# Performance work log

Measured on AMD Instinct MI355X. Metric: run time of the kernel, lower is better.

The kernel has to match this reference:

```python
import jax, jax.numpy as jnp
import numpy as np

N_OUT = 8      # outer experts
INNER = 2      # inner experts per outer expert
E = N_OUT * INNER  # 16 total experts
ACTI = 2       # outer top-k (acti_num)
PATTERN = (2, 1)   # inner top-k per outer slot (acti_pattern)
D = 1024       # hidden_dim
F = 512        # expert ffn dim
B, S = 1, 1024


def setup_inputs() -> dict:
    key = jax.random.key(0)
    ks = jax.random.split(key, 6)
    w = lambda k, shape: jax.random.normal(k, shape, jnp.float32) * 0.02
    return {
        "hidden_states": jax.random.normal(ks[0], (B, S, D), jnp.float32),
        "w_out_gate": w(ks[1], (N_OUT, D)),
        "w_in_gates": w(ks[2], (N_OUT, INNER, D)),
        "w_gate_proj": w(ks[3], (E, F, D)),
        "w_up_proj": w(ks[4], (E, F, D)),
        "w_down_proj": w(ks[5], (E, D, F)),
    }


def reference(hidden_states, w_out_gate, w_in_gates, w_gate_proj, w_up_proj, w_down_proj):
    Bb, Ss, Dd = hidden_states.shape
    x = hidden_states.reshape(-1, Dd)          # [T, D]
    T = x.shape[0]

    # --- RouterCompound: outer gate ---
    logits = x @ w_out_gate.T                  # [T, n_out]
    probs = jax.nn.softmax(logits.astype(jnp.float32), axis=-1)
    rw, sel = jax.lax.top_k(probs, ACTI)       # [T, A] weights, outer expert ids
    rw = rw / rw.sum(axis=-1, keepdims=True)   # norm_topk_prob=True

    # --- inner gates: score all (outer, inner) pairs, gather selected outer ---
    inner_all = jnp.einsum('td,oid->toi', x, w_in_gates)           # [T, n_out, inner]
    inner_sel = jnp.take_along_axis(inner_all, sel[:, :, None], axis=1)  # [T, A, inner]
    max_k = max(PATTERN)
    _, top_idx = jax.lax.top_k(inner_sel, max_k)                   # [T, A, max_k]
    flat_ids = sel[:, :, None] * INNER + top_idx                   # global expert ids
    # per outer slot j keep first PATTERN[j] inner experts (static pattern)
    sel_ids = jnp.concatenate([flat_ids[:, j, :p] for j, p in enumerate(PATTERN)], axis=1)  # [T, K]
    sel_w = jnp.concatenate([jnp.repeat(rw[:, j:j + 1], p, axis=1) for j, p in enumerate(PATTERN)], axis=1)  # [T, K]
    sel_w = sel_w.astype(x.dtype)

    # --- dispatch/combine: dense masked combine (math-identical to index_add loop) ---
    combine = jnp.zeros((T, E), x.dtype).at[jnp.arange(T)[:, None], sel_ids].add(sel_w)  # [T, E]
    g = jnp.einsum('td,efd->tef', x, w_gate_proj)   # [T, E, F]
    u = jnp.einsum('td,efd->tef', x, w_up_proj)
    h = jax.nn.silu(g) * u                          # SwiGLU activation
    y = jnp.einsum('tef,edf->ted', h, w_down_proj)  # [T, E, D]
    out = jnp.einsum('ted,te->td', y, combine)      # weighted combine
    return out.reshape(Bb, Ss, Dd), sel_w
```

## Files before the change

kernel.cpp:

```cpp
#include <hip/hip_runtime.h>
#include <hip/hip_bf16.h>

typedef __bf16 bf16_t;
typedef __bf16 bf16x8 __attribute__((ext_vector_type(8)));
typedef float floatx4 __attribute__((ext_vector_type(4)));
typedef unsigned int u32;

#define T_TOK 1024
#define DIM   1024
#define FF    512
#define NEXP  16

#define FLAG_OFF 0
#define CNT_OFF  64
#define TOK_OFF  256
#define SEL_OFF  65792
#define H_OFF    78080
#define XBF_OFF  (H_OFF + (size_t)3072*512*2)
#define WGB_OFF  (XBF_OFF + (size_t)T_TOK*DIM*2)
#define WUB_OFF  (WGB_OFF + (size_t)NEXP*FF*DIM*2)
#define WDB_OFF  (WUB_OFF + (size_t)NEXP*FF*DIM*2)
#define Y_OFF    (WDB_OFF + (size_t)NEXP*DIM*FF*2)
#define WS_FULL  (Y_OFF + (size_t)3072*DIM*4)

__device__ inline float swiglu(float g, float u) {
    float a = fminf(fmaxf(-g, -60.f), 60.f);
    return g * u / (1.0f + __expf(a));
}

__device__ __forceinline__ void gload_lds16(const void* g, void* l) {
    __builtin_amdgcn_global_load_lds((const __attribute__((address_space(1))) u32*)g,
                                     (__attribute__((address_space(3))) u32*)l, 16, 0, 0);
}

template<int N> __device__ __forceinline__ void waitv() {
    asm volatile("s_waitcnt vmcnt(%0)" :: "n"(N) : "memory");
}
__device__ __forceinline__ void barrier_raw() { __builtin_amdgcn_s_barrier(); }

__device__ __forceinline__ bf16x8 cvt8(float4 a, float4 b) {
    bf16x8 r;
    r[0]=(bf16_t)a.x; r[1]=(bf16_t)a.y; r[2]=(bf16_t)a.z; r[3]=(bf16_t)a.w;
    r[4]=(bf16_t)b.x; r[5]=(bf16_t)b.y; r[6]=(bf16_t)b.z; r[7]=(bf16_t)b.w;
    return r;
}

__device__ __forceinline__ bf16x8 rdT(const char* L, int r, int q) {
    return *(const bf16x8*)(L + r * 128 + ((q ^ (r & 7)) << 4));
}

__device__ inline bf16x8 loadB8r(const void* base, size_t off, bool f32) {
    if (f32) {
        const float4* p = (const float4*)((const float*)base + off);
        return cvt8(p[0], p[1]);
    } else {
        return *(const bf16x8*)((const bf16_t*)base + off);
    }
}

__device__ int blk_f32(const void* p, int tid, int* tmp) {
    const unsigned short* h = (const unsigned short*)p;
    unsigned bad = 0;
    for (int i = tid; i < 4096; i += 256) {
        unsigned e = ((unsigned)h[i] >> 7) & 0xFFu;
        if (e >= 0x90u) bad = 1;
    }
    unsigned long long bl = __ballot(bad != 0);
    __syncthreads();
    if ((tid & 63) == 0) tmp[tid >> 6] = (bl != 0ull) ? 1 : 0;
    __syncthreads();
    return tmp[0] | tmp[1] | tmp[2] | tmp[3];
}

__global__ __launch_bounds__(256) void prep2_kernel(
    const void* __restrict__ x, const void* __restrict__ w_out, const void* __restrict__ w_in,
    const void* __restrict__ wg, const void* __restrict__ wu, const void* __restrict__ wd,
    float* __restrict__ selw_out, int* __restrict__ sel_ids,
    bf16_t* __restrict__ xb, int* __restrict__ flags,
    bf16_t* __restrict__ wgb, bf16_t* __restrict__ wub, bf16_t* __restrict__ wdb)
{
    const int b = blockIdx.x;
    const int tid = threadIdx.x;
    __shared__ int tmp[4];
    __shared__ float Ls[24];

    if (b >= T_TOK + 6) {
        const int c = b - (T_TOK + 6);
        const int z = c >> 12, i = c & 4095;
        const void* src; bf16_t* dst;
        if (z == 0)      { src = wg; dst = wgb; }
        else if (z == 1) { src = wu; dst = wub; }
        else             { src = wd; dst = wdb; }
        const unsigned short* h = (const unsigned short*)src;
        unsigned bad = 0;
        for (int k = tid; k < 4096; k += 256) {
            unsigned ex = ((unsigned)h[k] >> 7) & 0xFFu;
            if (ex >= 0x90u) bad = 1;
        }
        unsigned long long bl = __ballot(bad != 0);
        if ((tid & 63) == 0) tmp[tid >> 6] = (bl != 0ull) ? 1 : 0;
        __syncthreads();
        if (!(tmp[0] | tmp[1] | tmp[2] | tmp[3])) return;
        size_t off = ((size_t)i * 256 + tid) * 8;
        const float4* p = (const float4*)((const float*)src + off);
        float4 a = p[0], bb = p[1];
        *(bf16x8*)(dst + off) = cvt8(a, bb);
        return;
    }

    if (b >= T_TOK) {
        const int j = b - T_TOK;
        const void* ps[6] = {x, w_out, w_in, wg, wu, wd};
        const unsigned short* h = (const unsigned short*)ps[j];
        unsigned bad = 0;
        for (int i = tid; i < 4096; i += 256) {
            unsigned e = ((unsigned)h[i] >> 7) & 0xFFu;
            if (e >= 0x90u) bad = 1;
        }
        unsigned long long bl = __ballot(bad != 0);
        if ((tid & 63) == 0) tmp[tid >> 6] = (bl != 0ull) ? 1 : 0;
        __syncthreads();
        if (tid == 0) flags[j] = tmp[0] | tmp[1] | tmp[2] | tmp[3];
        return;
    }

    const bool xf  = blk_f32(x, tid, tmp) != 0;
    const bool gof = blk_f32(w_out, tid, tmp) != 0;
    const bool gif = blk_f32(w_in, tid, tmp) != 0;

    const int wave = tid >> 6, lane = tid & 63;
    const int t = b;

    float xv[16];
    if (xf) {
        const float* xp = (const float*)x + (size_t)t * DIM;
        #pragma unroll
        for (int i = 0; i < 16; i++) xv[i] = xp[lane + 64 * i];
    } else {
        const bf16_t* xp = (const bf16_t*)x + (size_t)t * DIM;
        #pragma unroll
        for (int i = 0; i < 16; i++) xv[i] = (float)xp[lane + 64 * i];
    }

    if (wave == 0 && xb) {
        #pragma unroll
        for (int i = 0; i < 16; i++)
            xb[(size_t)t * DIM + lane + 64 * i] = (bf16_t)xv[i];
    }

    #pragma unroll
    for (int jj = 0; jj < 6; jj++) {
        const int j = wave * 6 + jj;
        const void* gb; int row; bool gf;
        if (j < 8) { gb = w_out; row = j;     gf = gof; }
        else       { gb = w_in;  row = j - 8; gf = gif; }
        float s = 0.f;
        if (gf) {
            const float* gp = (const float*)gb + (size_t)row * DIM;
            #pragma unroll
            for (int i = 0; i < 16; i++) s += xv[i] * gp[lane + 64 * i];
        } else {
            const bf16_t* gp = (const bf16_t*)gb + (size_t)row * DIM;
            #pragma unroll
            for (int i = 0; i < 16; i++) s += xv[i] * (float)gp[lane + 64 * i];
        }
        #pragma unroll
        for (int m = 32; m >= 1; m >>= 1) s += __shfl_xor(s, m, 64);
        if (lane == 0) Ls[j] = s;
    }
    __syncthreads();

    if (tid == 0) {
        const float* logits = Ls;
        float mx = logits[0];
        for (int o = 1; o < 8; o++) mx = fmaxf(mx, logits[o]);
        float p[8];
        for (int o = 0; o < 8; o++) p[o] = __expf(logits[o] - mx);
        int i0 = 0;
        for (int o = 1; o < 8; o++) if (logits[o] > logits[i0]) i0 = o;
        int i1 = (i0 == 0) ? 1 : 0;
        for (int o = 0; o < 8; o++) if (o != i0 && logits[o] > logits[i1]) i1 = o;
        float rsum = p[i0] + p[i1];
        float rw0 = p[i0] / rsum, rw1 = p[i1] / rsum;

        float a0 = logits[8 + i0 * 2], a1 = logits[8 + i0 * 2 + 1];
        int j00 = (a1 > a0) ? 1 : 0;
        float b0 = logits[8 + i1 * 2], b1 = logits[8 + i1 * 2 + 1];
        int j10 = (b1 > b0) ? 1 : 0;

        int   ids[3] = { i0 * 2 + j00, i0 * 2 + (1 - j00), i1 * 2 + j10 };
        float w[3]   = { rw0, rw0, rw1 };

        #pragma unroll
        for (int k = 0; k < 3; k++) {
            selw_out[t * 3 + k] = w[k];
            sel_ids[t * 3 + k]  = ids[k];
        }
    }
}

__global__ __launch_bounds__(1024) void bin2_kernel(
    const int* __restrict__ sel_ids,
    int* __restrict__ cnt, int* __restrict__ tok_enc)
{
    const int e = blockIdx.x, tid = threadIdx.x;
    const int wave = tid >> 6, lane = tid & 63;
    __shared__ int wbase[16];

    int my = -1;
    #pragma unroll
    for (int k = 0; k < 3; k++) {
        int id = sel_ids[tid * 3 + k];
        if (id == e) my = tid | (k << 16);
    }
    unsigned long long b = __ballot(my >= 0);
    if (lane == 0) wbase[wave] = __popcll(b);
    __syncthreads();
    if (tid == 0) {
        int s = 0;
        for (int w = 0; w < 16; w++) { int c = wbase[w]; wbase[w] = s; s += c; }
        cnt[e] = s;
    }
    __syncthreads();
    if (my >= 0) {
        int pos = wbase[wave] + __popcll(b & ((1ull << lane) - 1ull));
        if (pos < T_TOK) tok_enc[e * T_TOK + pos] = my;
    }
}


__global__ __launch_bounds__(512, 4) void gateup5_kernel(
    const bf16_t* __restrict__ xb,
    const void* __restrict__ wg, const void* __restrict__ wu,
    const bf16_t* __restrict__ wgb, const bf16_t* __restrict__ wub,
    const int* __restrict__ flags, const int* __restrict__ cnt,
    const int* __restrict__ tok_enc, bf16_t* __restrict__ H)
{
    __shared__ __align__(16) char Xs[3 * 16384];
    __shared__ __align__(16) char Gs[3 * 4096];
    __shared__ __align__(16) char Us[3 * 4096];
    __shared__ int toks[128];
    __shared__ int hrow[128];

    const int ft = blockIdx.x, mt = blockIdx.y, e = blockIdx.z;
    int C = cnt[e]; if (C > T_TOK) C = T_TOK; if (C < 0) C = 0;
    if (mt * 128 >= C) return;

    const bf16_t* wgp = (flags[3] != 0) ? wgb : (const bf16_t*)wg;
    const bf16_t* wup = (flags[4] != 0) ? wub : (const bf16_t*)wu;

    const int tid = threadIdx.x;
    if (tid < 128) {
        int idx = mt * 128 + tid, t = 0, hr = -1;
        if (idx < C) {
            int enc = tok_enc[e * T_TOK + idx];
            int tt = enc & 0xFFFF, kk = (enc >> 16) & 0xFFFF;
            if (tt < T_TOK && kk < 3) { t = tt; hr = tt * 3 + kk; }
        }
        toks[tid] = t; hrow[tid] = hr;
    }
    __syncthreads();

    const int wave = tid >> 6, lane = tid & 63;
    const int mh = wave >> 1, fq = wave & 1;
    const int rsel = lane & 15, kq = lane >> 4;

    constexpr int NC  = 16;
    constexpr int PER = 3;

    const bf16_t* px[2];
    #pragma unroll
    for (int j = 0; j < 2; j++) {
        int n = (2 * wave + j) * 64 + lane, r = n >> 3, s = n & 7;
        px[j] = xb + (size_t)toks[r] * DIM + ((s ^ (r & 7)) << 3);
    }
    const bf16_t* pw;
    {
        int wv = wave & 3;
        int n = wv * 64 + lane, r = n >> 3, s = n & 7;
        int row = e * FF + ft * 32 + r;
        pw = (wave < 4 ? wgp : wup) + (size_t)row * DIM + ((s ^ (r & 7)) << 3);
    }
    char* wdst = (wave < 4 ? Gs : Us);
    const int wslot = (wave & 3) * 1024;

    auto issue = [&](int kc) {
        const int buf = kc % 3;
        gload_lds16(px[0] + kc * 64, Xs + buf * 16384 + (2 * wave) * 1024);
        gload_lds16(px[1] + kc * 64, Xs + buf * 16384 + (2 * wave + 1) * 1024);
        gload_lds16(pw + kc * 64, wdst + buf * 4096 + wslot);
    };

    floatx4 ag[2], au[2];
    #pragma unroll
    for (int ms = 0; ms < 2; ms++) { ag[ms] = (floatx4){0,0,0,0}; au[ms] = (floatx4){0,0,0,0}; }

    issue(0);
    issue(1);

    #pragma unroll
    for (int kc = 0; kc < NC; kc++) {
        if (kc + 2 < NC) issue(kc + 2);
        if (kc + 2 < NC)      waitv<2 * PER>();
        else if (kc + 1 < NC) waitv<PER>();
        else                  waitv<0>();
        barrier_raw();
        __builtin_amdgcn_sched_barrier(0);

        const char* X = Xs + (kc % 3) * 16384;
        const char* G = Gs + (kc % 3) * 4096;
        const char* U = Us + (kc % 3) * 4096;
        #pragma unroll
        for (int i = 0; i < 2; i++) {
            const int q = i * 4 + kq;
            bf16x8 a0 = rdT(X, mh * 32 + rsel, q);
            bf16x8 a1 = rdT(X, mh * 32 + 16 + rsel, q);
            bf16x8 bg = rdT(G, fq * 16 + rsel, q);
            bf16x8 bu = rdT(U, fq * 16 + rsel, q);
            ag[0] = __builtin_amdgcn_mfma_f32_16x16x32_bf16(a0, bg, ag[0], 0, 0, 0);
            au[0] = __builtin_amdgcn_mfma_f32_16x16x32_bf16(a0, bu, au[0], 0, 0, 0);
            ag[1] = __builtin_amdgcn_mfma_f32_16x16x32_bf16(a1, bg, ag[1], 0, 0, 0);
            au[1] = __builtin_amdgcn_mfma_f32_16x16x32_bf16(a1, bu, au[1], 0, 0, 0);
        }
        barrier_raw();
    }

    const int f = ft * 32 + fq * 16 + rsel;
    #pragma unroll
    for (int ms = 0; ms < 2; ms++)
        #pragma unroll
        for (int r = 0; r < 4; r++) {
            int m = mh * 32 + ms * 16 + kq * 4 + r;
            int hr = hrow[m];
            if (hr >= 0)
                H[(size_t)hr * FF + f] = (bf16_t)swiglu(ag[ms][r], au[ms][r]);
        }
}

__global__ __launch_bounds__(512, 4) void down5_kernel(
    const void* __restrict__ wd, const bf16_t* __restrict__ wdb,
    const int* __restrict__ flags, const int* __restrict__ cnt,
    const int* __restrict__ tok_enc,
    const bf16_t* __restrict__ H, float* __restrict__ Y)
{
    __shared__ __align__(16) char Hs[3 * 16384];
    __shared__ __align__(16) char Ds[3 * 8192];
    __shared__ int hsrc[128];
    __shared__ int hdst[128];

    const int dt = blockIdx.x, mt = blockIdx.y, e = blockIdx.z;
    int C = cnt[e]; if (C > T_TOK) C = T_TOK; if (C < 0) C = 0;
    if (mt * 128 >= C) return;

    const bf16_t* wdp = (flags[5] != 0) ? wdb : (const bf16_t*)wd;

    const int tid = threadIdx.x;
    if (tid < 128) {
        int idx = mt * 128 + tid, hr = -1;
        if (idx < C) {
            int enc = tok_enc[e * T_TOK + idx];
            int tt = enc & 0xFFFF, kk = (enc >> 16) & 0xFFFF;
            if (tt < T_TOK && kk < 3) hr = tt * 3 + kk;
        }
        hsrc[tid] = (hr >= 0) ? hr : 0;
        hdst[tid] = hr;
    }
    __syncthreads();

    const int wave = tid >> 6, lane = tid & 63;
    const int mh = wave >> 1, dq = wave & 1;
    const int rsel = lane & 15, kq = lane >> 4;

    constexpr int NC  = 8;
    constexpr int PER = 3;

    const bf16_t* ph[2];
    #pragma unroll
    for (int j = 0; j < 2; j++) {
        int n = (2 * wave + j) * 64 + lane, r = n >> 3, s = n & 7;
        ph[j] = H + (size_t)hsrc[r] * FF + ((s ^ (r & 7)) << 3);
    }
    const bf16_t* pd;
    {
        int n = wave * 64 + lane, r = n >> 3, s = n & 7;
        int row = e * DIM + dt * 64 + r;
        pd = wdp + (size_t)row * FF + ((s ^ (r & 7)) << 3);
    }

    auto issue = [&](int kc) {
        const int buf = kc % 3;
        gload_lds16(ph[0] + kc * 64, Hs + buf * 16384 + (2 * wave) * 1024);
        gload_lds16(ph[1] + kc * 64, Hs + buf * 16384 + (2 * wave + 1) * 1024);
        gload_lds16(pd + kc * 64, Ds + buf * 8192 + wave * 1024);
    };

    floatx4 acc[2][2];
    #pragma unroll
    for (int ms = 0; ms < 2; ms++)
        #pragma unroll
        for (int nt = 0; nt < 2; nt++) acc[ms][nt] = (floatx4){0,0,0,0};

    issue(0);
    issue(1);

    #pragma unroll
    for (int kc = 0; kc < NC; kc++) {
        if (kc + 2 < NC) issue(kc + 2);
        if (kc + 2 < NC)      waitv<2 * PER>();
        else if (kc + 1 < NC) waitv<PER>();
        else                  waitv<0>();
        barrier_raw();
        __builtin_amdgcn_sched_barrier(0);

        const char* Hb = Hs + (kc % 3) * 16384;
        const char* Db = Ds + (kc % 3) * 8192;
        #pragma unroll
        for (int i = 0; i < 2; i++) {
            const int q = i * 4 + kq;
            bf16x8 a0 = rdT(Hb, mh * 32 + rsel, q);
            bf16x8 a1 = rdT(Hb, mh * 32 + 16 + rsel, q);
            bf16x8 b0 = rdT(Db, dq * 32 + rsel, q);
            bf16x8 b1 = rdT(Db, dq * 32 + 16 + rsel, q);
            acc[0][0] = __builtin_amdgcn_mfma_f32_16x16x32_bf16(a0, b0, acc[0][0], 0, 0, 0);
            acc[0][1] = __builtin_amdgcn_mfma_f32_16x16x32_bf16(a0, b1, acc[0][1], 0, 0, 0);
            acc[1][0] = __builtin_amdgcn_mfma_f32_16x16x32_bf16(a1, b0, acc[1][0], 0, 0, 0);
            acc[1][1] = __builtin_amdgcn_mfma_f32_16x16x32_bf16(a1, b1, acc[1][1], 0, 0, 0);
        }
        barrier_raw();
    }

    #pragma unroll
    for (int ms = 0; ms < 2; ms++)
        #pragma unroll
        for (int nt = 0; nt < 2; nt++)
            #pragma unroll
            for (int r = 0; r < 4; r++) {
                int m = mh * 32 + ms * 16 + kq * 4 + r;
                int hr = hdst[m];
                if (hr >= 0)
                    Y[(size_t)hr * DIM + dt * 64 + dq * 32 + nt * 16 + rsel] = acc[ms][nt][r];
            }
}

__global__ __launch_bounds__(256) void combine_kernel(
    const float* __restrict__ Y, const float* __restrict__ selw,
    float* __restrict__ outp)
{
    int idx = blockIdx.x * 256 + threadIdx.x;
    int t = idx >> 8;
    int d = (idx & 255) * 4;
    float w0 = selw[t * 3 + 0], w1 = selw[t * 3 + 1], w2 = selw[t * 3 + 2];
    float4 y0 = *(const float4*)(Y + (size_t)(t * 3 + 0) * DIM + d);
    float4 y1 = *(const float4*)(Y + (size_t)(t * 3 + 1) * DIM + d);
    float4 y2 = *(const float4*)(Y + (size_t)(t * 3 + 2) * DIM + d);
    float4 o;
    o.x = w0 * y0.x + w1 * y1.x + w2 * y2.x;
    o.y = w0 * y0.y + w1 * y1.y + w2 * y2.y;
    o.z = w0 * y0.z + w1 * y1.z + w2 * y2.z;
    o.w = w0 * y0.w + w1 * y1.w + w2 * y2.w;
    *(float4*)(outp + (size_t)t * DIM + d) = o;
}

__global__ __launch_bounds__(256) void ffn_kernel(
    const void* __restrict__ x,
    const void* __restrict__ wg, const void* __restrict__ wu, const void* __restrict__ wd,
    const int* __restrict__ flags, const int* __restrict__ cnt, const int* __restrict__ tok_enc,
    const float* __restrict__ selw, float* __restrict__ outp)
{
    const int e = blockIdx.x, tile = blockIdx.y;
    int C = cnt[e]; if (C > T_TOK) C = T_TOK; if (C < 0) C = 0;
    if (tile * 16 >= C) return;
    const bool xf = flags[0] != 0, gf = flags[3] != 0, uf = flags[4] != 0, df = flags[5] != 0;

    __shared__ __align__(16) bf16_t Xs[16][1032];
    __shared__ __align__(16) bf16_t Hs[16][520];
    __shared__ int toks[16];
    __shared__ float wts[16];
    const int tid = threadIdx.x;
    if (tid < 16) {
        int idx = tile * 16 + tid, t = -1; float w = 0.f;
        if (idx < C) {
            int enc = tok_enc[e * T_TOK + idx];
            int tt = enc & 0xFFFF, kk = (enc >> 16) & 0xFFFF;
            if (tt < T_TOK && kk < 3) { t = tt; w = selw[tt * 3 + kk]; }
        }
        toks[tid] = t; wts[tid] = w;
    }
    __syncthreads();
    {
        int row = tid >> 4, chunk = tid & 15;
        int t = toks[row];
        bf16x8* dst = (bf16x8*)&Xs[row][chunk * 64];
        if (t >= 0) {
            #pragma unroll
            for (int i = 0; i < 8; i++)
                dst[i] = loadB8r(x, (size_t)t * DIM + chunk * 64 + i * 8, xf);
        } else {
            bf16x8 z;
            #pragma unroll
            for (int kz = 0; kz < 8; kz++) z[kz] = (bf16_t)0.0f;
            #pragma unroll
            for (int i = 0; i < 8; i++) dst[i] = z;
        }
    }
    __syncthreads();

    const int wave = tid >> 6, lane = tid & 63;
    const int rsel = lane & 15, kq = lane >> 4;
    const size_t eoffF = (size_t)e * FF * DIM;
    for (int nt = 0; nt < 8; nt++) {
        const int f0 = wave * 128 + nt * 16;
        const size_t boff = eoffF + (size_t)(f0 + rsel) * DIM + kq * 8;
        const bf16_t* ap = &Xs[rsel][kq * 8];
        floatx4 accg = {0.f,0.f,0.f,0.f};
        floatx4 accu = {0.f,0.f,0.f,0.f};
        for (int k0 = 0; k0 < DIM; k0 += 32) {
            bf16x8 a  = *(const bf16x8*)(ap + k0);
            bf16x8 bg = loadB8r(wg, boff + k0, gf);
            bf16x8 bu = loadB8r(wu, boff + k0, uf);
            accg = __builtin_amdgcn_mfma_f32_16x16x32_bf16(a, bg, accg, 0, 0, 0);
            accu = __builtin_amdgcn_mfma_f32_16x16x32_bf16(a, bu, accu, 0, 0, 0);
        }
        #pragma unroll
        for (int r = 0; r < 4; r++)
            Hs[kq * 4 + r][f0 + rsel] = (bf16_t)swiglu(accg[r], accu[r]);
    }
    __syncthreads();
    const size_t eoffD = (size_t)e * DIM * FF;
    for (int nt = 0; nt < 16; nt++) {
        const int d0 = wave * 256 + nt * 16;
        const size_t boff = eoffD + (size_t)(d0 + rsel) * FF + kq * 8;
        const bf16_t* ap = &Hs[rsel][kq * 8];
        floatx4 acc = {0.f,0.f,0.f,0.f};
        for (int k0 = 0; k0 < FF; k0 += 32) {
            bf16x8 a = *(const bf16x8*)(ap + k0);
            bf16x8 b = loadB8r(wd, boff + k0, df);
            acc = __builtin_amdgcn_mfma_f32_16x16x32_bf16(a, b, acc, 0, 0, 0);
        }
        #pragma unroll
        for (int r = 0; r < 4; r++) {
            int m = kq * 4 + r, t = toks[m];
            if (t >= 0) atomicAdd(outp + (size_t)t * DIM + d0 + rsel, acc[r] * wts[m]);
        }
    }
}

extern "C" void kernel_launch(void* const* d_in, const int* in_sizes, int n_in,
                              void* d_out, int out_size, void* d_ws, size_t ws_size,
                              hipStream_t stream)
{
    const void* x     = d_in[0];
    const void* w_out = d_in[1];
    const void* w_in  = d_in[2];
    const void* wg    = d_in[3];
    const void* wu    = d_in[4];
    const void* wd    = d_in[5];
    float* out  = (float*)d_out;
    float* selw = out + (size_t)T_TOK * DIM;

    char* ws = (char*)d_ws;
    int*    flags = (int*)(ws + FLAG_OFF);
    int*    cnt   = (int*)(ws + CNT_OFF);
    int*    tok   = (int*)(ws + TOK_OFF);
    int*    sel   = (int*)(ws + SEL_OFF);
    bf16_t* H     = (bf16_t*)(ws + H_OFF);
    bf16_t* xbf   = (bf16_t*)(ws + XBF_OFF);
    bf16_t* wgb   = (bf16_t*)(ws + WGB_OFF);
    bf16_t* wub   = (bf16_t*)(ws + WUB_OFF);
    bf16_t* wdb   = (bf16_t*)(ws + WDB_OFF);
    float*  Y     = (float*)(ws + Y_OFF);

    const bool full = ws_size >= (size_t)WS_FULL;

    if (!full)
        hipMemsetAsync(out, 0, (size_t)T_TOK * DIM * sizeof(float), stream);

    const int nblk = (T_TOK + 6) + (full ? 3 * 4096 : 0);
    prep2_kernel<<<dim3(nblk), dim3(256), 0, stream>>>(
        x, w_out, w_in, wg, wu, wd, selw, sel,
        full ? xbf : (bf16_t*)nullptr, flags, wgb, wub, wdb);

    bin2_kernel<<<dim3(NEXP), dim3(1024), 0, stream>>>(sel, cnt, tok);

    if (full) {
        gateup5_kernel<<<dim3(16, 8, 16), dim3(512), 0, stream>>>(
            xbf, wg, wu, wgb, wub, flags, cnt, tok, H);
        down5_kernel<<<dim3(16, 8, 16), dim3(512), 0, stream>>>(
            wd, wdb, flags, cnt, tok, H, Y);
        combine_kernel<<<dim3(T_TOK * DIM / 1024), dim3(256), 0, stream>>>(Y, selw, out);
    } else {
        ffn_kernel<<<dim3(NEXP, 64), dim3(256), 0, stream>>>(
            x, wg, wu, wd, flags, cnt, tok, selw, out);
    }
}
```

Before: 191.8 us.

## Load fp32 expert weights directly into LDS and convert at fragment read time

Drops the separate pass that converted fp32 gate/up/down weights to bf16 copies in the workspace. The GEMM kernels now stream fp32 weights straight into LDS with a 16-way XOR swizzle and convert to bf16 while reading MFMA fragments, with the path picked per dtype through template specialisation. Pipelining goes from triple to double buffering to fit the larger fp32 tiles in LDS. Format detection moves into a small kernel of its own ahead of the router. This removes a full read and write of all weights each call, but gives up one stage of prefetch depth and adds conversion work inside the inner loop.

```diff
diff --git a/kernel.cpp b/kernel.cpp
--- a/kernel.cpp
+++ b/kernel.cpp
@@ -17,10 +17,7 @@
 #define SEL_OFF  65792
 #define H_OFF    78080
 #define XBF_OFF  (H_OFF + (size_t)3072*512*2)
-#define WGB_OFF  (XBF_OFF + (size_t)T_TOK*DIM*2)
-#define WUB_OFF  (WGB_OFF + (size_t)NEXP*FF*DIM*2)
-#define WDB_OFF  (WUB_OFF + (size_t)NEXP*FF*DIM*2)
-#define Y_OFF    (WDB_OFF + (size_t)NEXP*DIM*FF*2)
+#define Y_OFF    (XBF_OFF + (size_t)T_TOK*DIM*2)
 #define WS_FULL  (Y_OFF + (size_t)3072*DIM*4)
 
 __device__ inline float swiglu(float g, float u) {
@@ -47,6 +44,17 @@
 
 __device__ __forceinline__ bf16x8 rdT(const char* L, int r, int q) {
     return *(const bf16x8*)(L + r * 128 + ((q ^ (r & 7)) << 4));
+}
+template<bool F32>
+__device__ __forceinline__ bf16x8 rdW(const char* L, int r, int q) {
+    if constexpr (F32) {
+        const float* p = (const float*)(L + r * 256);
+        float4 a = *(const float4*)(p + ((((2 * q)    ) ^ (r & 15)) << 2));
+        float4 b = *(const float4*)(p + ((((2 * q) + 1) ^ (r & 15)) << 2));
+        return cvt8(a, b);
+    } else {
+        return *(const bf16x8*)(L + r * 128 + ((q ^ (r & 7)) << 4));
+    }
 }
 
 __device__ inline bf16x8 loadB8r(const void* base, size_t off, bool f32) {
@@ -58,78 +66,41 @@
     }
 }
 
-__device__ int blk_f32(const void* p, int tid, int* tmp) {
-    const unsigned short* h = (const unsigned short*)p;
-    unsigned bad = 0;
-    for (int i = tid; i < 4096; i += 256) {
-        unsigned e = ((unsigned)h[i] >> 7) & 0xFFu;
+__global__ __launch_bounds__(64) void detect_kernel(
+    const void* p0, const void* p1, const void* p2,
+    const void* p3, const void* p4, const void* p5,
+    int* __restrict__ flags)
+{
+    const void* ps[6] = {p0, p1, p2, p3, p4, p5};
+    int j = blockIdx.x;
+    int lane = threadIdx.x;
+    const unsigned short* h = (const unsigned short*)ps[j];
+    unsigned int bad = 0;
+    for (int i = lane; i < 4096; i += 64) {
+        unsigned int e = ((unsigned int)h[i] >> 7) & 0xFFu;
         if (e >= 0x90u) bad = 1;
     }
-    unsigned long long bl = __ballot(bad != 0);
-    __syncthreads();
-    if ((tid & 63) == 0) tmp[tid >> 6] = (bl != 0ull) ? 1 : 0;
-    __syncthreads();
-    return tmp[0] | tmp[1] | tmp[2] | tmp[3];
-}
-
-__global__ __launch_bounds__(256) void prep2_kernel(
-    const void* __restrict__ x, const void* __restrict__ w_out, const void* __restrict__ w_in,
-    const void* __restrict__ wg, const void* __restrict__ wu, const void* __restrict__ wd,
-    float* __restrict__ selw_out, int* __restrict__ sel_ids,
-    bf16_t* __restrict__ xb, int* __restrict__ flags,
-    bf16_t* __restrict__ wgb, bf16_t* __restrict__ wub, bf16_t* __restrict__ wdb)
-{
-    const int b = blockIdx.x;
+    unsigned long long b = __ballot(bad);
+    if (lane == 0) flags[j] = (b != 0ull) ? 1 : 0;
+}
+
+__global__ __launch_bounds__(256) void router4_kernel(
+    const void* __restrict__ x,
+    const void* __restrict__ w_out,
+    const void* __restrict__ w_in,
+    float* __restrict__ selw_out,
+    const int* __restrict__ flags,
+    int* __restrict__ sel_ids,
+    bf16_t* __restrict__ xb)
+{
+    const bool xf  = flags[0] != 0;
+    const bool gof = flags[1] != 0;
+    const bool gif = flags[2] != 0;
     const int tid = threadIdx.x;
-    __shared__ int tmp[4];
+    const int wave = tid >> 6, lane = tid & 63;
+    const int t = blockIdx.x;
+
     __shared__ float Ls[24];
-
-    if (b >= T_TOK + 6) {
-        const int c = b - (T_TOK + 6);
-        const int z = c >> 12, i = c & 4095;
-        const void* src; bf16_t* dst;
-        if (z == 0)      { src = wg; dst = wgb; }
-        else if (z == 1) { src = wu; dst = wub; }
-        else             { src = wd; dst = wdb; }
-        const unsigned short* h = (const unsigned short*)src;
-        unsigned bad = 0;
-        for (int k = tid; k < 4096; k += 256) {
-            unsigned ex = ((unsigned)h[k] >> 7) & 0xFFu;
-            if (ex >= 0x90u) bad = 1;
-        }
-        unsigned long long bl = __ballot(bad != 0);
-        if ((tid & 63) == 0) tmp[tid >> 6] = (bl != 0ull) ? 1 : 0;
-        __syncthreads();
-        if (!(tmp[0] | tmp[1] | tmp[2] | tmp[3])) return;
-        size_t off = ((size_t)i * 256 + tid) * 8;
-        const float4* p = (const float4*)((const float*)src + off);
-        float4 a = p[0], bb = p[1];
-        *(bf16x8*)(dst + off) = cvt8(a, bb);
-        return;
-    }
-
-    if (b >= T_TOK) {
-        const int j = b - T_TOK;
-        const void* ps[6] = {x, w_out, w_in, wg, wu, wd};
-        const unsigned short* h = (const unsigned short*)ps[j];
-        unsigned bad = 0;
-        for (int i = tid; i < 4096; i += 256) {
-            unsigned e = ((unsigned)h[i] >> 7) & 0xFFu;
-            if (e >= 0x90u) bad = 1;
-        }
-        unsigned long long bl = __ballot(bad != 0);
-        if ((tid & 63) == 0) tmp[tid >> 6] = (bl != 0ull) ? 1 : 0;
-        __syncthreads();
-        if (tid == 0) flags[j] = tmp[0] | tmp[1] | tmp[2] | tmp[3];
-        return;
-    }
-
-    const bool xf  = blk_f32(x, tid, tmp) != 0;
-    const bool gof = blk_f32(w_out, tid, tmp) != 0;
-    const bool gif = blk_f32(w_in, tid, tmp) != 0;
-
-    const int wave = tid >> 6, lane = tid & 63;
-    const int t = b;
 
     float xv[16];
     if (xf) {
@@ -229,25 +200,17 @@
 }
 
 
-__global__ __launch_bounds__(512, 4) void gateup5_kernel(
+template<bool GF, bool UF>
+__device__ __forceinline__ void gateup6_body(
     const bf16_t* __restrict__ xb,
     const void* __restrict__ wg, const void* __restrict__ wu,
-    const bf16_t* __restrict__ wgb, const bf16_t* __restrict__ wub,
-    const int* __restrict__ flags, const int* __restrict__ cnt,
-    const int* __restrict__ tok_enc, bf16_t* __restrict__ H)
-{
-    __shared__ __align__(16) char Xs[3 * 16384];
-    __shared__ __align__(16) char Gs[3 * 4096];
-    __shared__ __align__(16) char Us[3 * 4096];
-    __shared__ int toks[128];
-    __shared__ int hrow[128];
-
+    const int* __restrict__ cnt, const int* __restrict__ tok_enc,
+    bf16_t* __restrict__ H,
+    char* Xs, char* Gs, char* Us, int* toks, int* hrow)
+{
     const int ft = blockIdx.x, mt = blockIdx.y, e = blockIdx.z;
     int C = cnt[e]; if (C > T_TOK) C = T_TOK; if (C < 0) C = 0;
     if (mt * 128 >= C) return;
-
-    const bf16_t* wgp = (flags[3] != 0) ? wgb : (const bf16_t*)wg;
-    const bf16_t* wup = (flags[4] != 0) ? wub : (const bf16_t*)wu;
 
     const int tid = threadIdx.x;
     if (tid < 128) {
@@ -265,8 +228,12 @@
     const int mh = wave >> 1, fq = wave & 1;
     const int rsel = lane & 15, kq = lane >> 4;
 
-    constexpr int NC  = 16;
-    constexpr int PER = 3;
+    constexpr int NC = 16;
+    constexpr int GSTR = GF ? 8192 : 4096;
+    constexpr int USTR = UF ? 8192 : 4096;
+    constexpr int PG = 2 + (GF ? 2 : 1);
+    constexpr int PU = 2 + (UF ? 2 : 1);
+    const int wrow0 = e * FF + ft * 32;
 
     const bf16_t* px[2];
     #pragma unroll
@@ -274,21 +241,50 @@
         int n = (2 * wave + j) * 64 + lane, r = n >> 3, s = n & 7;
         px[j] = xb + (size_t)toks[r] * DIM + ((s ^ (r & 7)) << 3);
     }
-    const bf16_t* pw;
-    {
-        int wv = wave & 3;
-        int n = wv * 64 + lane, r = n >> 3, s = n & 7;
-        int row = e * FF + ft * 32 + r;
-        pw = (wave < 4 ? wgp : wup) + (size_t)row * DIM + ((s ^ (r & 7)) << 3);
-    }
-    char* wdst = (wave < 4 ? Gs : Us);
-    const int wslot = (wave & 3) * 1024;
+    const int wv = wave & 3;
+    const void* pw0; const void* pw1 = nullptr;
+    char* wdst;
+    int woff0, woff1 = 0;
+    if (wave < 4) {
+        wdst = Gs;
+        if constexpr (GF) {
+            int n0 = (2 * wv) * 64 + lane, r0 = n0 >> 4, s0 = n0 & 15;
+            int n1 = (2 * wv + 1) * 64 + lane, r1 = n1 >> 4, s1 = n1 & 15;
+            pw0 = (const float*)wg + (size_t)(wrow0 + r0) * DIM + ((s0 ^ (r0 & 15)) << 2);
+            pw1 = (const float*)wg + (size_t)(wrow0 + r1) * DIM + ((s1 ^ (r1 & 15)) << 2);
+            woff0 = (2 * wv) * 1024; woff1 = (2 * wv + 1) * 1024;
+        } else {
+            int n = wv * 64 + lane, r = n >> 3, s = n & 7;
+            pw0 = (const bf16_t*)wg + (size_t)(wrow0 + r) * DIM + ((s ^ (r & 7)) << 3);
+            woff0 = wv * 1024;
+        }
+    } else {
+        wdst = Us;
+        if constexpr (UF) {
+            int n0 = (2 * wv) * 64 + lane, r0 = n0 >> 4, s0 = n0 & 15;
+            int n1 = (2 * wv + 1) * 64 + lane, r1 = n1 >> 4, s1 = n1 & 15;
+            pw0 = (const float*)wu + (size_t)(wrow0 + r0) * DIM + ((s0 ^ (r0 & 15)) << 2);
+            pw1 = (const float*)wu + (size_t)(wrow0 + r1) * DIM + ((s1 ^ (r1 & 15)) << 2);
+            woff0 = (2 * wv) * 1024; woff1 = (2 * wv + 1) * 1024;
+        } else {
+            int n = wv * 64 + lane, r = n >> 3, s = n & 7;
+            pw0 = (const bf16_t*)wu + (size_t)(wrow0 + r) * DIM + ((s ^ (r & 7)) << 3);
+            woff0 = wv * 1024;
+        }
+    }
+    const bool wf = (wave < 4) ? GF : UF;
+    const int wstr = (wave < 4) ? GSTR : USTR;
 
     auto issue = [&](int kc) {
-        const int buf = kc % 3;
+        const int buf = kc & 1;
         gload_lds16(px[0] + kc * 64, Xs + buf * 16384 + (2 * wave) * 1024);
         gload_lds16(px[1] + kc * 64, Xs + buf * 16384 + (2 * wave + 1) * 1024);
-        gload_lds16(pw + kc * 64, wdst + buf * 4096 + wslot);
+        if (wf) {
+            gload_lds16((const float*)pw0 + kc * 64, wdst + buf * wstr + woff0);
+            gload_lds16((const float*)pw1 + kc * 64, wdst + buf * wstr + woff1);
+        } else {
+            gload_lds16((const bf16_t*)pw0 + kc * 64, wdst + buf * wstr + woff0);
+        }
     };
 
     floatx4 ag[2], au[2];
@@ -296,27 +292,28 @@
     for (int ms = 0; ms < 2; ms++) { ag[ms] = (floatx4){0,0,0,0}; au[ms] = (floatx4){0,0,0,0}; }
 
     issue(0);
-    issue(1);
 
     #pragma unroll
     for (int kc = 0; kc < NC; kc++) {
-        if (kc + 2 < NC) issue(kc + 2);
-        if (kc + 2 < NC)      waitv<2 * PER>();
-        else if (kc + 1 < NC) waitv<PER>();
-        else                  waitv<0>();
+        if (kc + 1 < NC) {
+            issue(kc + 1);
+            if (wave < 4) waitv<PG>(); else waitv<PU>();
+        } else {
+            waitv<0>();
+        }
         barrier_raw();
         __builtin_amdgcn_sched_barrier(0);
 
-        const char* X = Xs + (kc % 3) * 16384;
-        const char* G = Gs + (kc % 3) * 4096;
-        const char* U = Us + (kc % 3) * 4096;
+        const char* X = Xs + (kc & 1) * 16384;
+        const char* G = Gs + (kc & 1) * GSTR;
+        const char* U = Us + (kc & 1) * USTR;
         #pragma unroll
         for (int i = 0; i < 2; i++) {
             const int q = i * 4 + kq;
             bf16x8 a0 = rdT(X, mh * 32 + rsel, q);
             bf16x8 a1 = rdT(X, mh * 32 + 16 + rsel, q);
-            bf16x8 bg = rdT(G, fq * 16 + rsel, q);
-            bf16x8 bu = rdT(U, fq * 16 + rsel, q);
+            bf16x8 bg = rdW<GF>(G, fq * 16 + rsel, q);
+            bf16x8 bu = rdW<UF>(U, fq * 16 + rsel, q);
             ag[0] = __builtin_amdgcn_mfma_f32_16x16x32_bf16(a0, bg, ag[0], 0, 0, 0);
             au[0] = __builtin_amdgcn_mfma_f32_16x16x32_bf16(a0, bu, au[0], 0, 0, 0);
             ag[1] = __builtin_amdgcn_mfma_f32_16x16x32_bf16(a1, bg, ag[1], 0, 0, 0);
@@ -337,22 +334,37 @@
         }
 }
 
-__global__ __launch_bounds__(512, 4) void down5_kernel(
-    const void* __restrict__ wd, const bf16_t* __restrict__ wdb,
+__global__ __launch_bounds__(512, 4) void gateup6_kernel(
+    const bf16_t* __restrict__ xb,
+    const void* __restrict__ wg, const void* __restrict__ wu,
     const int* __restrict__ flags, const int* __restrict__ cnt,
-    const int* __restrict__ tok_enc,
-    const bf16_t* __restrict__ H, float* __restrict__ Y)
-{
-    __shared__ __align__(16) char Hs[3 * 16384];
-    __shared__ __align__(16) char Ds[3 * 8192];
-    __shared__ int hsrc[128];
-    __shared__ int hdst[128];
-
+    const int* __restrict__ tok_enc, bf16_t* __restrict__ H)
+{
+    __shared__ __align__(16) char Xs[2 * 16384];
+    __shared__ __align__(16) char Gs[2 * 8192];
+    __shared__ __align__(16) char Us[2 * 8192];
+    __shared__ int toks[128];
+    __shared__ int hrow[128];
+    const bool gf = flags[3] != 0, uf = flags[4] != 0;
+    if (gf) {
+        if (uf) gateup6_body<true,  true >(xb, wg, wu, cnt, tok_enc, H, Xs, Gs, Us, toks, hrow);
+        else    gateup6_body<true,  false>(xb, wg, wu, cnt, tok_enc, H, Xs, Gs, Us, toks, hrow);
+    } else {
+        if (uf) gateup6_body<false, true >(xb, wg, wu, cnt, tok_enc, H, Xs, Gs, Us, toks, hrow);
+        else    gateup6_body<false, false>(xb, wg, wu, cnt, tok_enc, H, Xs, Gs, Us, toks, hrow);
+    }
+}
+
+template<bool DF>
+__device__ __forceinline__ void down6_body(
+    const void* __restrict__ wd,
+    const int* __restrict__ cnt, const int* __restrict__ tok_enc,
+    const bf16_t* __restrict__ H, float* __restrict__ Y,
+    char* Hs, char* Ds, int* hsrc, int* hdst)
+{
     const int dt = blockIdx.x, mt = blockIdx.y, e = blockIdx.z;
     int C = cnt[e]; if (C > T_TOK) C = T_TOK; if (C < 0) C = 0;
     if (mt * 128 >= C) return;
-
-    const bf16_t* wdp = (flags[5] != 0) ? wdb : (const bf16_t*)wd;
 
     const int tid = threadIdx.x;
     if (tid < 128) {
@@ -371,8 +383,10 @@
     const int mh = wave >> 1, dq = wave & 1;
     const int rsel = lane & 15, kq = lane >> 4;
 
-    constexpr int NC  = 8;
-    constexpr int PER = 3;
+    constexpr int NC = 8;
+    constexpr int DSTR = DF ? 16384 : 8192;
+    constexpr int PER = 2 + (DF ? 2 : 1);
+    const int wrow0 = e * DIM + dt * 64;
 
     const bf16_t* ph[2];
     #pragma unroll
@@ -380,18 +394,30 @@
         int n = (2 * wave + j) * 64 + lane, r = n >> 3, s = n & 7;
         ph[j] = H + (size_t)hsrc[r] * FF + ((s ^ (r & 7)) << 3);
     }
-    const bf16_t* pd;
-    {
+    const void* pd0; const void* pd1 = nullptr;
+    int doff0, doff1 = 0;
+    if constexpr (DF) {
+        int n0 = (2 * wave) * 64 + lane, r0 = n0 >> 4, s0 = n0 & 15;
+        int n1 = (2 * wave + 1) * 64 + lane, r1 = n1 >> 4, s1 = n1 & 15;
+        pd0 = (const float*)wd + (size_t)(wrow0 + r0) * FF + ((s0 ^ (r0 & 15)) << 2);
+        pd1 = (const float*)wd + (size_t)(wrow0 + r1) * FF + ((s1 ^ (r1 & 15)) << 2);
+        doff0 = (2 * wave) * 1024; doff1 = (2 * wave + 1) * 1024;
+    } else {
         int n = wave * 64 + lane, r = n >> 3, s = n & 7;
-        int row = e * DIM + dt * 64 + r;
-        pd = wdp + (size_t)row * FF + ((s ^ (r & 7)) << 3);
+        pd0 = (const bf16_t*)wd + (size_t)(wrow0 + r) * FF + ((s ^ (r & 7)) << 3);
+        doff0 = wave * 1024;
     }
 
     auto issue = [&](int kc) {
-        const int buf = kc % 3;
+        const int buf = kc & 1;
         gload_lds16(ph[0] + kc * 64, Hs + buf * 16384 + (2 * wave) * 1024);
         gload_lds16(ph[1] + kc * 64, Hs + buf * 16384 + (2 * wave + 1) * 1024);
-        gload_lds16(pd + kc * 64, Ds + buf * 8192 + wave * 1024);
+        if constexpr (DF) {
+            gload_lds16((const float*)pd0 + kc * 64, Ds + buf * DSTR + doff0);
+            gload_lds16((const float*)pd1 + kc * 64, Ds + buf * DSTR + doff1);
+        } else {
+            gload_lds16((const bf16_t*)pd0 + kc * 64, Ds + buf * DSTR + doff0);
+        }
     };
 
     floatx4 acc[2][2];
@@ -401,26 +427,23 @@
         for (int nt = 0; nt < 2; nt++) acc[ms][nt] = (floatx4){0,0,0,0};
 
     issue(0);
-    issue(1);
 
     #pragma unroll
     for (int kc = 0; kc < NC; kc++) {
-        if (kc + 2 < NC) issue(kc + 2);
-        if (kc + 2 < NC)      waitv<2 * PER>();
-        else if (kc + 1 < NC) waitv<PER>();
-        else                  waitv<0>();
+        if (kc + 1 < NC) { issue(kc + 1); waitv<PER>(); }
+        else             { waitv<0>(); }
         barrier_raw();
         __builtin_amdgcn_sched_barrier(0);
 
-        const char* Hb = Hs + (kc % 3) * 16384;
-        const char* Db = Ds + (kc % 3) * 8192;
+        const char* Hb = Hs + (kc & 1) * 16384;
+        const char* Db = Ds + (kc & 1) * DSTR;
         #pragma unroll
         for (int i = 0; i < 2; i++) {
             const int q = i * 4 + kq;
             bf16x8 a0 = rdT(Hb, mh * 32 + rsel, q);
             bf16x8 a1 = rdT(Hb, mh * 32 + 16 + rsel, q);
-            bf16x8 b0 = rdT(Db, dq * 32 + rsel, q);
-            bf16x8 b1 = rdT(Db, dq * 32 + 16 + rsel, q);
+            bf16x8 b0 = rdW<DF>(Db, dq * 32 + rsel, q);
+            bf16x8 b1 = rdW<DF>(Db, dq * 32 + 16 + rsel, q);
             acc[0][0] = __builtin_amdgcn_mfma_f32_16x16x32_bf16(a0, b0, acc[0][0], 0, 0, 0);
             acc[0][1] = __builtin_amdgcn_mfma_f32_16x16x32_bf16(a0, b1, acc[0][1], 0, 0, 0);
             acc[1][0] = __builtin_amdgcn_mfma_f32_16x16x32_bf16(a1, b0, acc[1][0], 0, 0, 0);
@@ -440,6 +463,21 @@
                 if (hr >= 0)
                     Y[(size_t)hr * DIM + dt * 64 + dq * 32 + nt * 16 + rsel] = acc[ms][nt][r];
             }
+}
+
+__global__ __launch_bounds__(512, 4) void down6_kernel(
+    const void* __restrict__ wd,
+    const int* __restrict__ flags, const int* __restrict__ cnt,
+    const int* __restrict__ tok_enc,
+    const bf16_t* __restrict__ H, float* __restrict__ Y)
+{
+    __shared__ __align__(16) char Hs[2 * 16384];
+    __shared__ __align__(16) char Ds[2 * 16384];
+    __shared__ int hsrc[128];
+    __shared__ int hdst[128];
+    const bool df = flags[5] != 0;
+    if (df) down6_body<true >(wd, cnt, tok_enc, H, Y, Hs, Ds, hsrc, hdst);
+    else    down6_body<false>(wd, cnt, tok_enc, H, Y, Hs, Ds, hsrc, hdst);
 }
 
 __global__ __launch_bounds__(256) void combine_kernel(
@@ -565,9 +603,6 @@
     int*    sel   = (int*)(ws + SEL_OFF);
     bf16_t* H     = (bf16_t*)(ws + H_OFF);
     bf16_t* xbf   = (bf16_t*)(ws + XBF_OFF);
-    bf16_t* wgb   = (bf16_t*)(ws + WGB_OFF);
-    bf16_t* wub   = (bf16_t*)(ws + WUB_OFF);
-    bf16_t* wdb   = (bf16_t*)(ws + WDB_OFF);
     float*  Y     = (float*)(ws + Y_OFF);
 
     const bool full = ws_size >= (size_t)WS_FULL;
@@ -575,18 +610,18 @@
     if (!full)
         hipMemsetAsync(out, 0, (size_t)T_TOK * DIM * sizeof(float), stream);
 
-    const int nblk = (T_TOK + 6) + (full ? 3 * 4096 : 0);
-    prep2_kernel<<<dim3(nblk), dim3(256), 0, stream>>>(
-        x, w_out, w_in, wg, wu, wd, selw, sel,
-        full ? xbf : (bf16_t*)nullptr, flags, wgb, wub, wdb);
+    detect_kernel<<<dim3(6), dim3(64), 0, stream>>>(x, w_out, w_in, wg, wu, wd, flags);
+
+    router4_kernel<<<dim3(T_TOK), dim3(256), 0, stream>>>(
+        x, w_out, w_in, selw, flags, sel, full ? xbf : (bf16_t*)nullptr);
 
     bin2_kernel<<<dim3(NEXP), dim3(1024), 0, stream>>>(sel, cnt, tok);
 
     if (full) {
-        gateup5_kernel<<<dim3(16, 8, 16), dim3(512), 0, stream>>>(
-            xbf, wg, wu, wgb, wub, flags, cnt, tok, H);
-        down5_kernel<<<dim3(16, 8, 16), dim3(512), 0, stream>>>(
-            wd, wdb, flags, cnt, tok, H, Y);
+        gateup6_kernel<<<dim3(16, 8, 16), dim3(512), 0, stream>>>(
+            xbf, wg, wu, flags, cnt, tok, H);
+        down6_kernel<<<dim3(16, 8, 16), dim3(512), 0, stream>>>(
+            wd, flags, cnt, tok, H, Y);
         combine_kernel<<<dim3(T_TOK * DIM / 1024), dim3(256), 0, stream>>>(Y, selw, out);
     } else {
         ffn_kernel<<<dim3(NEXP, 64), dim3(256), 0, stream>>>(
```

After: 187.1 us. 1.03x faster.
